# Kernel optimization log

Hardware: AMD Instinct MI355X
Metric: run time of the kernel (lower is better)

## Reference

```python
import jax, jax.numpy as jnp
import numpy as np

N = 4096        # number of sparse voxel tokens (single sequence)
C = 1024        # channels
H = 16          # num_heads
D = C // H      # head_dim = 64
FREQ_DIM = D // 2 // 3   # 10 rotary freqs per spatial axis
PAD = D // 2 - 3 * FREQ_DIM  # 2 identity-padded complex pairs


def setup_inputs() -> dict:
    key = jax.random.key(0)
    ks = jax.random.split(key, 6)
    s_in = 1.0 / np.sqrt(C)
    x = jax.random.normal(ks[0], (N, C), jnp.float32)
    coords = jax.random.randint(ks[1], (N, 3), 0, 64, dtype=jnp.int32)
    W_qkv = jax.random.normal(ks[2], (C, 3 * C), jnp.float32) * s_in
    b_qkv = jnp.zeros((3 * C,), jnp.float32)
    gamma_q = jnp.ones((H, D), jnp.float32)
    gamma_k = jnp.ones((H, D), jnp.float32)
    W_out = jax.random.normal(ks[3], (C, C), jnp.float32) * s_in
    b_out = jnp.zeros((C,), jnp.float32)
    return {"x": x, "coords": coords, "W_qkv": W_qkv, "b_qkv": b_qkv,
            "gamma_q": gamma_q, "gamma_k": gamma_k, "W_out": W_out, "b_out": b_out}


def _rms_norm(t, gamma):
    # F.normalize(x, dim=-1) * gamma * sqrt(D), computed in fp32
    t = t.astype(jnp.float32)
    nrm = jnp.maximum(jnp.linalg.norm(t, axis=-1, keepdims=True), 1e-12)
    return (t / nrm) * gamma * np.float32(np.sqrt(D))


def _rope_phases(coords):
    # freqs: rope_freq[0] / rope_freq[1]**(i/freq_dim)
    freqs = 1.0 / (10000.0 ** (jnp.arange(FREQ_DIM, dtype=jnp.float32) / FREQ_DIM))
    ph = coords.astype(jnp.float32).reshape(-1)[:, None] * freqs   # [N*3, FREQ_DIM]
    ph = ph.reshape(N, 3 * FREQ_DIM)
    # pad with zero-phase (identity rotation) to head_dim//2
    cos = jnp.concatenate([jnp.cos(ph), jnp.ones((N, PAD), jnp.float32)], axis=-1)
    sin = jnp.concatenate([jnp.sin(ph), jnp.zeros((N, PAD), jnp.float32)], axis=-1)
    return cos, sin


def _rope_apply(t, cos, sin):
    # complex rotation on consecutive pairs of the head dim
    tr = t.reshape(N, H, D // 2, 2)
    t0, t1 = tr[..., 0], tr[..., 1]
    c, s = cos[:, None, :], sin[:, None, :]
    o0 = t0 * c - t1 * s
    o1 = t0 * s + t1 * c
    return jnp.stack([o0, o1], axis=-1).reshape(N, H, D)


def reference(x, coords, W_qkv, b_qkv, gamma_q, gamma_k, W_out, b_out):
    qkv = (x @ W_qkv + b_qkv).reshape(N, 3, H, D)
    q, k, v = qkv[:, 0], qkv[:, 1], qkv[:, 2]
    q = _rms_norm(q, gamma_q)
    k = _rms_norm(k, gamma_k)
    cos, sin = _rope_phases(coords)
    q = _rope_apply(q, cos, sin)
    k = _rope_apply(k, cos, sin)
    scores = jnp.einsum('nhd,mhd->hnm', q, k) / np.float32(np.sqrt(D))
    attn = jax.nn.softmax(scores, axis=-1)
    h = jnp.einsum('hnm,mhd->nhd', attn, v).reshape(N, C)
    return h @ W_out + b_out
```

## Files before the change

### kernel.cpp

```cpp
#include <hip/hip_runtime.h>

#define DEVI __device__ __forceinline__

typedef __attribute__((ext_vector_type(8))) short bf16x8;
typedef __attribute__((ext_vector_type(4))) float f32x4;
typedef __attribute__((ext_vector_type(16))) float f32x16;

DEVI ushort f2bf(float f) {
  union { float f; unsigned u; } v; v.f = f;
  unsigned u = v.u;
  unsigned r = (u + 0x7FFFu + ((u >> 16) & 1u)) >> 16;
  return (ushort)r;
}
DEVI float bf2f(ushort h) {
  union { unsigned u; float f; } v; v.u = ((unsigned)h) << 16;
  return v.f;
}
DEVI unsigned pkbf(float lo, float hi) {
  unsigned r;
  asm("v_cvt_pk_bf16_f32 %0, %1, %2" : "=v"(r) : "v"(lo), "v"(hi));
  return r;
}
DEVI float exp2v(float x) {
#if __has_builtin(__builtin_amdgcn_exp2f)
  return __builtin_amdgcn_exp2f(x);
#else
  return exp2f(x);
#endif
}

DEVI void gload_lds16(const ushort* g, ushort* l) {
  __builtin_amdgcn_global_load_lds((const __attribute__((address_space(1))) void*)g,
                                   (__attribute__((address_space(3))) void*)l, 16, 0, 0);
}

DEVI void xcd_swz(int& bx, int& by) {
  const int nx = gridDim.x;
  const int flat = blockIdx.x + blockIdx.y * nx;
  const int cpx = (nx * gridDim.y) >> 3;
  const int swz = (flat & 7) * cpx + (flat >> 3);
  bx = swz % nx;
  by = swz / nx;
}

__global__ __launch_bounds__(256) void prep(const float* __restrict__ x,
                                            ushort* __restrict__ xb,
                                            const float* __restrict__ Wq,
                                            ushort* __restrict__ wtq,
                                            const float* __restrict__ Wo,
                                            ushort* __restrict__ wto) {
  __shared__ ushort tile[64][65];
  const int bid = blockIdx.x, t = threadIdx.x;
  if (bid < 4096) {
    int i = bid * 256 + t;
    const float4 v = ((const float4*)x)[i];
    uint2 o;
    o.x = (unsigned)f2bf(v.x) | ((unsigned)f2bf(v.y) << 16);
    o.y = (unsigned)f2bf(v.z) | ((unsigned)f2bf(v.w) << 16);
    ((uint2*)xb)[i] = o;
    return;
  }
  const float* in;
  ushort* out;
  int R, Cc, bx, by;
  if (bid < 4864) {
    in = Wq; out = wtq; R = 1024; Cc = 3072;
    bx = (bid - 4096) % 48; by = (bid - 4096) / 48;
  } else {
    in = Wo; out = wto; R = 1024; Cc = 1024;
    bx = (bid - 4864) % 16; by = (bid - 4864) / 16;
  }
  const int r0 = by * 64, c0 = bx * 64;
  for (int i = 0; i < 16; ++i) {
    int rr = i * 4 + (t >> 6), cc = t & 63;
    tile[rr][cc] = f2bf(in[(size_t)(r0 + rr) * Cc + c0 + cc]);
  }
  __syncthreads();
  for (int i = 0; i < 16; ++i) {
    int cc = i * 4 + (t >> 6), rr = t & 63;
    out[(size_t)(c0 + cc) * R + r0 + rr] = tile[rr][cc];
  }
}

template<int EPI>
__global__ __launch_bounds__(256) void gemm_bt(const ushort* __restrict__ A,
                                               const ushort* __restrict__ Bt,
                                               const float* __restrict__ bias,
                                               void* __restrict__ outp,
                                               int M, int Nn, int K) {
  __shared__ ushort As[2][128 * 32];
  __shared__ ushort Bs[2][128 * 32];
  const int tid = threadIdx.x;
  const int w = tid >> 6, l = tid & 63;
  int bx, by;
  xcd_swz(bx, by);
  const int m0 = by * 128, n0 = bx * 128;
  const int wm = (w >> 1) * 64, wn = (w & 1) * 64;
  const int lc = l & 15, lg = l >> 4;

  f32x4 acc[4][4];
  for (int i = 0; i < 4; ++i)
    for (int j = 0; j < 4; ++j) acc[i][j] = (f32x4){0.f, 0.f, 0.f, 0.f};

  const int srow = w * 32 + (l >> 2);
  const int scol = (l & 3) * 8;
  const ushort* gA = A + (size_t)(m0 + srow) * K + scol;
  const ushort* gB = Bt + (size_t)(n0 + srow) * K + scol;

  for (int k0 = 0; k0 < K; k0 += 64) {
#pragma unroll
    for (int s = 0; s < 2; ++s) {
      gload_lds16(gA + k0 + 32 * s,                  &As[s][(w * 32 + 0) * 32]);
      gload_lds16(gA + k0 + 32 * s + (size_t)16 * K, &As[s][(w * 32 + 16) * 32]);
      gload_lds16(gB + k0 + 32 * s,                  &Bs[s][(w * 32 + 0) * 32]);
      gload_lds16(gB + k0 + 32 * s + (size_t)16 * K, &Bs[s][(w * 32 + 16) * 32]);
    }
    __syncthreads();
#pragma unroll
    for (int s = 0; s < 2; ++s) {
      bf16x8 af[4], bfr[4];
      for (int mi = 0; mi < 4; ++mi)
        af[mi] = *(const bf16x8*)(&As[s][(wm + mi * 16 + lc) * 32 + lg * 8]);
      for (int ni = 0; ni < 4; ++ni)
        bfr[ni] = *(const bf16x8*)(&Bs[s][(wn + ni * 16 + lc) * 32 + lg * 8]);
      for (int mi = 0; mi < 4; ++mi)
        for (int ni = 0; ni < 4; ++ni)
          acc[mi][ni] = __builtin_amdgcn_mfma_f32_16x16x32_bf16(af[mi], bfr[ni], acc[mi][ni], 0, 0, 0);
    }
    __syncthreads();
  }

  const int lr = lg * 4;
  if constexpr (EPI == 1) {
    float* O = (float*)outp;
    for (int ni = 0; ni < 4; ++ni) {
      int col = n0 + wn + ni * 16 + lc;
      float bv = bias[col];
      for (int mi = 0; mi < 4; ++mi)
        for (int r = 0; r < 4; ++r)
          O[(size_t)(m0 + wm + mi * 16 + lr + r) * Nn + col] = acc[mi][ni][r] + bv;
    }
  } else {
    ushort* O = (ushort*)outp;
    for (int ni = 0; ni < 4; ++ni) {
      int col = n0 + wn + ni * 16 + lc;
      float bv = bias[col];
      int grp = col >> 10;
      int hh = (col >> 6) & 15;
      int dd = col & 63;
      if (grp < 2) {
        size_t base = (size_t)grp * (16 * 4096 * 64) + (size_t)hh * (4096 * 64) + dd;
        for (int mi = 0; mi < 4; ++mi)
          for (int r = 0; r < 4; ++r) {
            int row = m0 + wm + mi * 16 + lr + r;
            O[base + (size_t)row * 64] = f2bf(acc[mi][ni][r] + bv);
          }
      } else {
        size_t base = (size_t)2 * (16 * 4096 * 64) + ((size_t)hh * 64 + dd) * 4096;
        for (int mi = 0; mi < 4; ++mi)
          for (int r = 0; r < 4; ++r) {
            int row = m0 + wm + mi * 16 + lr + r;
            O[base + row] = f2bf(acc[mi][ni][r] + bv);
          }
      }
    }
  }
}

DEVI void nr_one(ushort* B, const float* g, size_t base, int h, int l16,
                 float c0a, float s0a, float c1a, float s1a, float extra) {
  unsigned u0 = *(const unsigned*)(B + base + 2 * l16);
  unsigned u1 = *(const unsigned*)(B + base + 32 + 2 * l16);
  float t00 = bf2f((ushort)u0), t01 = bf2f((ushort)(u0 >> 16));
  float t10 = bf2f((ushort)u1), t11 = bf2f((ushort)(u1 >> 16));
  float ss = t00 * t00 + t01 * t01 + t10 * t10 + t11 * t11;
  for (int d = 1; d < 16; d <<= 1) ss += __shfl_xor(ss, d, 16);
  float scl = 8.f / fmaxf(sqrtf(ss), 1e-12f);
  scl *= extra;
  float g00 = g[h * 64 + 2 * l16], g01 = g[h * 64 + 2 * l16 + 1];
  float g10 = g[h * 64 + 32 + 2 * l16], g11 = g[h * 64 + 33 + 2 * l16];
  float q00 = t00 * scl * g00, q01 = t01 * scl * g01;
  float q10 = t10 * scl * g10, q11 = t11 * scl * g11;
  float o00 = q00 * c0a - q01 * s0a, o01 = q00 * s0a + q01 * c0a;
  float o10 = q10 * c1a - q11 * s1a, o11 = q10 * s1a + q11 * c1a;
  *(unsigned*)(B + base + 2 * l16) = (unsigned)f2bf(o00) | ((unsigned)f2bf(o01) << 16);
  *(unsigned*)(B + base + 32 + 2 * l16) = (unsigned)f2bf(o10) | ((unsigned)f2bf(o11) << 16);
}

__global__ __launch_bounds__(256) void norm_rope(ushort* __restrict__ Qb,
                                                 ushort* __restrict__ Kb,
                                                 const int* __restrict__ coords,
                                                 const float* __restrict__ gq,
                                                 const float* __restrict__ gk) {
  const int n = blockIdx.x, t = threadIdx.x;
  const int h = t >> 4, l16 = t & 15;
  const float L2_10K_D10 = 1.3287712379549449f;
  float c0a, s0a, c1a, s1a;
  {
    int p = l16;
    int j = p / 10, fi = p - j * 10;
    float freq = exp2f(-(float)fi * L2_10K_D10);
    float ang = (float)coords[n * 3 + j] * freq;
    c0a = cosf(ang); s0a = sinf(ang);
  }
  {
    int p = l16 + 16;
    if (p < 30) {
      int j = p / 10, fi = p - j * 10;
      float freq = exp2f(-(float)fi * L2_10K_D10);
      float ang = (float)coords[n * 3 + j] * freq;
      c1a = cosf(ang); s1a = sinf(ang);
    } else { c1a = 1.f; s1a = 0.f; }
  }
  const size_t base = ((size_t)h * 4096 + n) * 64;
  nr_one(Qb, gq, base, h, l16, c0a, s0a, c1a, s1a, 0.125f * 1.4426950408889634f);
  nr_one(Kb, gk, base, h, l16, c0a, s0a, c1a, s1a, 1.0f);
}

DEVI void attn_step(const bf16x8 (&ck)[8], const bf16x8 (&cv)[8], const bf16x8 (&qf)[4],
                    f32x16& o0, f32x16& o1, f32x4& rs) {
  f32x16 s0, s1;
#pragma unroll
  for (int r = 0; r < 16; ++r) { s0[r] = 0.f; s1[r] = 0.f; }
#pragma unroll
  for (int c = 0; c < 4; ++c) {
    s0 = __builtin_amdgcn_mfma_f32_32x32x16_bf16(ck[c],     qf[c], s0, 0, 0, 0);
    s1 = __builtin_amdgcn_mfma_f32_32x32x16_bf16(ck[c + 4], qf[c], s1, 0, 0, 0);
  }
#pragma unroll
  for (int r = 0; r < 16; ++r) { s0[r] = exp2v(s0[r]); }
#pragma unroll
  for (int r = 0; r < 16; ++r) { s1[r] = exp2v(s1[r]); }
#pragma unroll
  for (int r = 0; r < 16; r += 4) {
    rs[0] += s0[r] + s1[r];
    rs[1] += s0[r + 1] + s1[r + 1];
    rs[2] += s0[r + 2] + s1[r + 2];
    rs[3] += s0[r + 3] + s1[r + 3];
  }
  union { unsigned u[4]; bf16x8 v; } pb[4];
  {
    auto r0 = __builtin_amdgcn_permlane32_swap(pkbf(s0[0], s0[1]), pkbf(s0[4], s0[5]), false, false);
    auto r1 = __builtin_amdgcn_permlane32_swap(pkbf(s0[2], s0[3]), pkbf(s0[6], s0[7]), false, false);
    pb[0].u[0] = r0[0]; pb[0].u[1] = r1[0]; pb[0].u[2] = r0[1]; pb[0].u[3] = r1[1];
    auto r2 = __builtin_amdgcn_permlane32_swap(pkbf(s0[8], s0[9]), pkbf(s0[12], s0[13]), false, false);
    auto r3 = __builtin_amdgcn_permlane32_swap(pkbf(s0[10], s0[11]), pkbf(s0[14], s0[15]), false, false);
    pb[1].u[0] = r2[0]; pb[1].u[1] = r3[0]; pb[1].u[2] = r2[1]; pb[1].u[3] = r3[1];
    auto r4 = __builtin_amdgcn_permlane32_swap(pkbf(s1[0], s1[1]), pkbf(s1[4], s1[5]), false, false);
    auto r5 = __builtin_amdgcn_permlane32_swap(pkbf(s1[2], s1[3]), pkbf(s1[6], s1[7]), false, false);
    pb[2].u[0] = r4[0]; pb[2].u[1] = r5[0]; pb[2].u[2] = r4[1]; pb[2].u[3] = r5[1];
    auto r6 = __builtin_amdgcn_permlane32_swap(pkbf(s1[8], s1[9]), pkbf(s1[12], s1[13]), false, false);
    auto r7 = __builtin_amdgcn_permlane32_swap(pkbf(s1[10], s1[11]), pkbf(s1[14], s1[15]), false, false);
    pb[3].u[0] = r6[0]; pb[3].u[1] = r7[0]; pb[3].u[2] = r6[1]; pb[3].u[3] = r7[1];
  }
#pragma unroll
  for (int c = 0; c < 4; ++c) {
    o0 = __builtin_amdgcn_mfma_f32_32x32x16_bf16(cv[c],     pb[c].v, o0, 0, 0, 0);
    o1 = __builtin_amdgcn_mfma_f32_32x32x16_bf16(cv[c + 4], pb[c].v, o1, 0, 0, 0);
  }
}

__global__ __launch_bounds__(256, 2) void attn_fwd(const ushort* __restrict__ Qb,
                                                   const ushort* __restrict__ Kb,
                                                   const ushort* __restrict__ Vt,
                                                   ushort* __restrict__ attnb) {
  __shared__ ushort Ks[2][4096];
  __shared__ ushort Vs[2][4096];

  const int flat = blockIdx.x + (blockIdx.y << 5);
  const int swz = (flat & 7) * 64 + (flat >> 3);
  const int bx = swz & 31, h = swz >> 5;

  const int l = threadIdx.x & 63, w = threadIdx.x >> 6;
  const int q = l & 31, hi = l >> 5;
  const int q0 = bx * 128 + w * 32;

  const ushort* qrow = Qb + ((size_t)h * 4096 + q0 + q) * 64 + hi * 8;
  bf16x8 qf[4];
#pragma unroll
  for (int c = 0; c < 4; ++c) qf[c] = *(const bf16x8*)(qrow + 16 * c);

  f32x16 o0, o1;
#pragma unroll
  for (int r = 0; r < 16; ++r) { o0[r] = 0.f; o1[r] = 0.f; }
  f32x4 rs = (f32x4){0.f, 0.f, 0.f, 0.f};

  const ushort* gK = Kb + ((size_t)h * 4096 + l) * 64 + 2 * w * 8;
  const ushort* gV = Vt + ((size_t)h * 64 + l) * 4096 + 2 * w * 8;

  ushort* Kc = &Ks[0][0]; ushort* Vc = &Vs[0][0];
  ushort* Kn = &Ks[1][0]; ushort* Vn = &Vs[1][0];

  gload_lds16(gK, Kc + 2 * w * 512);
  gload_lds16(gK + 8, Kc + (2 * w + 1) * 512);
  gload_lds16(gV, Vc + 2 * w * 512);
  gload_lds16(gV + 8, Vc + (2 * w + 1) * 512);
  asm volatile("s_waitcnt vmcnt(0)" ::: "memory");
  __builtin_amdgcn_s_barrier();
  __builtin_amdgcn_sched_barrier(0);

  const int lbase = hi * 512 + q * 8;
  for (int t = 0; t < 63; ++t) {
    const ushort* sK = gK + (size_t)(t + 1) * 64 * 64;
    const ushort* sV = gV + (t + 1) * 64;
    gload_lds16(sK, Kn + 2 * w * 512);
    gload_lds16(sK + 8, Kn + (2 * w + 1) * 512);
    gload_lds16(sV, Vn + 2 * w * 512);
    gload_lds16(sV + 8, Vn + (2 * w + 1) * 512);

    bf16x8 k[8], v[8];
#pragma unroll
    for (int c = 0; c < 4; ++c) {
      k[c]     = *(const bf16x8*)(Kc + lbase + c * 1024);
      k[c + 4] = *(const bf16x8*)(Kc + lbase + c * 1024 + 256);
      v[c]     = *(const bf16x8*)(Vc + lbase + c * 1024);
      v[c + 4] = *(const bf16x8*)(Vc + lbase + c * 1024 + 256);
    }
    __builtin_amdgcn_s_setprio(1);
    attn_step(k, v, qf, o0, o1, rs);
    __builtin_amdgcn_s_setprio(0);

    asm volatile("s_waitcnt vmcnt(0) lgkmcnt(0)" ::: "memory");
    __builtin_amdgcn_s_barrier();
    __builtin_amdgcn_sched_barrier(0);
    ushort* tp;
    tp = Kc; Kc = Kn; Kn = tp;
    tp = Vc; Vc = Vn; Vn = tp;
  }
  {
    bf16x8 k[8], v[8];
#pragma unroll
    for (int c = 0; c < 4; ++c) {
      k[c]     = *(const bf16x8*)(Kc + lbase + c * 1024);
      k[c + 4] = *(const bf16x8*)(Kc + lbase + c * 1024 + 256);
      v[c]     = *(const bf16x8*)(Vc + lbase + c * 1024);
      v[c + 4] = *(const bf16x8*)(Vc + lbase + c * 1024 + 256);
    }
    attn_step(k, v, qf, o0, o1, rs);
  }

  float lsum = (rs[0] + rs[1]) + (rs[2] + rs[3]);
  lsum += __shfl_xor(lsum, 32);
  const float inv = 1.f / lsum;
  ushort* orow = attnb + (size_t)(q0 + q) * 1024 + h * 64;
#pragma unroll
  for (int dt = 0; dt < 2; ++dt) {
    const f32x16& oo = dt ? o1 : o0;
#pragma unroll
    for (int g = 0; g < 4; ++g)
#pragma unroll
      for (int p2 = 0; p2 < 2; ++p2) {
        int r = g * 4 + p2 * 2;
        unsigned pk = pkbf(oo[r] * inv, oo[r + 1] * inv);
        *(unsigned*)(orow + dt * 32 + g * 8 + 4 * hi + p2 * 2) = pk;
      }
  }
}

extern "C" void kernel_launch(void* const* d_in, const int* in_sizes, int n_in,
                              void* d_out, int out_size, void* d_ws, size_t ws_size,
                              hipStream_t stream) {
  const float* x      = (const float*)d_in[0];
  const int*   coords = (const int*)d_in[1];
  const float* W_qkv  = (const float*)d_in[2];
  const float* b_qkv  = (const float*)d_in[3];
  const float* gq     = (const float*)d_in[4];
  const float* gk     = (const float*)d_in[5];
  const float* W_out  = (const float*)d_in[6];
  const float* b_out  = (const float*)d_in[7];
  float* out = (float*)d_out;

  char* ws = (char*)d_ws;
  ushort* xb    = (ushort*)(ws);
  ushort* wtqkv = (ushort*)(ws + (8u << 20));
  ushort* wtout = (ushort*)(ws + (14u << 20));
  ushort* Qb    = (ushort*)(ws + (16u << 20));
  ushort* Kb    = (ushort*)(ws + (24u << 20));
  ushort* Vt    = (ushort*)(ws + (32u << 20));
  ushort* attnb = (ushort*)(ws + (40u << 20));

  prep<<<5120, 256, 0, stream>>>(x, xb, W_qkv, wtqkv, W_out, wtout);
  gemm_bt<0><<<dim3(24, 32), 256, 0, stream>>>(xb, wtqkv, b_qkv, (void*)Qb, 4096, 3072, 1024);
  norm_rope<<<4096, 256, 0, stream>>>(Qb, Kb, coords, gq, gk);
  attn_fwd<<<dim3(32, 16), 256, 0, stream>>>(Qb, Kb, Vt, attnb);
  gemm_bt<1><<<dim3(8, 32), 256, 0, stream>>>(attnb, wtout, b_out, (void*)out, 4096, 1024, 1024);
}
```

Baseline: 158.6 us.

## Fuse QK RMS-norm and RoPE into QKV GEMM epilogue

Removes the separate norm_rope kernel and applies RMS normalization, gamma, softmax scale and rotary embedding inside the QKV GEMM epilogue. Each wave's 64-column tile covers exactly one head, so the per-row sum of squares is reduced with 16-lane shuffles and RoPE pairs are exchanged with a lane xor. This saves a kernel launch and a full read and write of Q and K. In exchange the epilogue recomputes sin/cos per element, loads coords per row, and adds more shuffles and register pressure to the GEMM.

```diff
diff --git a/kernel.cpp b/kernel.cpp
--- a/kernel.cpp
+++ b/kernel.cpp
@@ -87,7 +87,10 @@
                                                const ushort* __restrict__ Bt,
                                                const float* __restrict__ bias,
                                                void* __restrict__ outp,
-                                               int M, int Nn, int K) {
+                                               int M, int Nn, int K,
+                                               const int* __restrict__ coords,
+                                               const float* __restrict__ gq,
+                                               const float* __restrict__ gk) {
   __shared__ ushort As[2][128 * 32];
   __shared__ ushort Bs[2][128 * 32];
   const int tid = threadIdx.x;
@@ -142,79 +145,68 @@
     }
   } else {
     ushort* O = (ushort*)outp;
-    for (int ni = 0; ni < 4; ++ni) {
-      int col = n0 + wn + ni * 16 + lc;
-      float bv = bias[col];
-      int grp = col >> 10;
-      int hh = (col >> 6) & 15;
-      int dd = col & 63;
-      if (grp < 2) {
-        size_t base = (size_t)grp * (16 * 4096 * 64) + (size_t)hh * (4096 * 64) + dd;
-        for (int mi = 0; mi < 4; ++mi)
-          for (int r = 0; r < 4; ++r) {
-            int row = m0 + wm + mi * 16 + lr + r;
-            O[base + (size_t)row * 64] = f2bf(acc[mi][ni][r] + bv);
+    const int col0 = n0 + wn;
+    const int grp = col0 >> 10;
+    const int hh = (col0 >> 6) & 15;
+    if (grp < 2) {
+      const float extra = (grp == 0) ? 0.125f * 1.4426950408889634f : 1.0f;
+      const float* g = (grp == 0) ? gq : gk;
+      const float L2_10K_D10 = 1.3287712379549449f;
+      float gam[4], bv[4], cfreq[4];
+      int cj[4];
+#pragma unroll
+      for (int ni = 0; ni < 4; ++ni) {
+        gam[ni] = g[hh * 64 + ni * 16 + lc];
+        bv[ni] = bias[col0 + ni * 16 + lc];
+        int p = ni * 8 + (lc >> 1);
+        int j = p / 10, fi = p - 10 * j;
+        cj[ni] = j;
+        cfreq[ni] = (p < 30) ? exp2f(-(float)fi * L2_10K_D10) : 0.f;
+      }
+      const size_t hbase = (size_t)grp * (16 * 4096 * 64) + (size_t)hh * (4096 * 64);
+#pragma unroll
+      for (int mi = 0; mi < 4; ++mi)
+#pragma unroll
+        for (int r = 0; r < 4; ++r) {
+          const int row = m0 + wm + mi * 16 + lr + r;
+          float v[4];
+          float ss = 0.f;
+#pragma unroll
+          for (int ni = 0; ni < 4; ++ni) {
+            v[ni] = acc[mi][ni][r] + bv[ni];
+            ss += v[ni] * v[ni];
           }
-      } else {
+          ss += __shfl_xor(ss, 1, 16);
+          ss += __shfl_xor(ss, 2, 16);
+          ss += __shfl_xor(ss, 4, 16);
+          ss += __shfl_xor(ss, 8, 16);
+          const float scl = extra * 8.f / fmaxf(sqrtf(ss), 1e-12f);
+          const int c0 = coords[row * 3], c1 = coords[row * 3 + 1], c2 = coords[row * 3 + 2];
+#pragma unroll
+          for (int ni = 0; ni < 4; ++ni) {
+            float te = v[ni] * scl * gam[ni];
+            float po = __shfl_xor(te, 1);
+            int cc = cj[ni] == 0 ? c0 : (cj[ni] == 1 ? c1 : c2);
+            float ang = (float)cc * cfreq[ni];
+            float cs = cosf(ang), sn = sinf(ang);
+            float outv = (lc & 1) ? po * sn + te * cs : te * cs - po * sn;
+            O[hbase + (size_t)row * 64 + ni * 16 + lc] = f2bf(outv);
+          }
+        }
+    } else {
+      for (int ni = 0; ni < 4; ++ni) {
+        int col = col0 + ni * 16 + lc;
+        float bvv = bias[col];
+        int dd = col & 63;
         size_t base = (size_t)2 * (16 * 4096 * 64) + ((size_t)hh * 64 + dd) * 4096;
         for (int mi = 0; mi < 4; ++mi)
           for (int r = 0; r < 4; ++r) {
             int row = m0 + wm + mi * 16 + lr + r;
-            O[base + row] = f2bf(acc[mi][ni][r] + bv);
+            O[base + row] = f2bf(acc[mi][ni][r] + bvv);
           }
       }
     }
   }
-}
-
-DEVI void nr_one(ushort* B, const float* g, size_t base, int h, int l16,
-                 float c0a, float s0a, float c1a, float s1a, float extra) {
-  unsigned u0 = *(const unsigned*)(B + base + 2 * l16);
-  unsigned u1 = *(const unsigned*)(B + base + 32 + 2 * l16);
-  float t00 = bf2f((ushort)u0), t01 = bf2f((ushort)(u0 >> 16));
-  float t10 = bf2f((ushort)u1), t11 = bf2f((ushort)(u1 >> 16));
-  float ss = t00 * t00 + t01 * t01 + t10 * t10 + t11 * t11;
-  for (int d = 1; d < 16; d <<= 1) ss += __shfl_xor(ss, d, 16);
-  float scl = 8.f / fmaxf(sqrtf(ss), 1e-12f);
-  scl *= extra;
-  float g00 = g[h * 64 + 2 * l16], g01 = g[h * 64 + 2 * l16 + 1];
-  float g10 = g[h * 64 + 32 + 2 * l16], g11 = g[h * 64 + 33 + 2 * l16];
-  float q00 = t00 * scl * g00, q01 = t01 * scl * g01;
-  float q10 = t10 * scl * g10, q11 = t11 * scl * g11;
-  float o00 = q00 * c0a - q01 * s0a, o01 = q00 * s0a + q01 * c0a;
-  float o10 = q10 * c1a - q11 * s1a, o11 = q10 * s1a + q11 * c1a;
-  *(unsigned*)(B + base + 2 * l16) = (unsigned)f2bf(o00) | ((unsigned)f2bf(o01) << 16);
-  *(unsigned*)(B + base + 32 + 2 * l16) = (unsigned)f2bf(o10) | ((unsigned)f2bf(o11) << 16);
-}
-
-__global__ __launch_bounds__(256) void norm_rope(ushort* __restrict__ Qb,
-                                                 ushort* __restrict__ Kb,
-                                                 const int* __restrict__ coords,
-                                                 const float* __restrict__ gq,
-                                                 const float* __restrict__ gk) {
-  const int n = blockIdx.x, t = threadIdx.x;
-  const int h = t >> 4, l16 = t & 15;
-  const float L2_10K_D10 = 1.3287712379549449f;
-  float c0a, s0a, c1a, s1a;
-  {
-    int p = l16;
-    int j = p / 10, fi = p - j * 10;
-    float freq = exp2f(-(float)fi * L2_10K_D10);
-    float ang = (float)coords[n * 3 + j] * freq;
-    c0a = cosf(ang); s0a = sinf(ang);
-  }
-  {
-    int p = l16 + 16;
-    if (p < 30) {
-      int j = p / 10, fi = p - j * 10;
-      float freq = exp2f(-(float)fi * L2_10K_D10);
-      float ang = (float)coords[n * 3 + j] * freq;
-      c1a = cosf(ang); s1a = sinf(ang);
-    } else { c1a = 1.f; s1a = 0.f; }
-  }
-  const size_t base = ((size_t)h * 4096 + n) * 64;
-  nr_one(Qb, gq, base, h, l16, c0a, s0a, c1a, s1a, 0.125f * 1.4426950408889634f);
-  nr_one(Kb, gk, base, h, l16, c0a, s0a, c1a, s1a, 1.0f);
 }
 
 DEVI void attn_step(const bf16x8 (&ck)[8], const bf16x8 (&cv)[8], const bf16x8 (&qf)[4],
@@ -380,8 +372,9 @@
   ushort* attnb = (ushort*)(ws + (40u << 20));
 
   prep<<<5120, 256, 0, stream>>>(x, xb, W_qkv, wtqkv, W_out, wtout);
-  gemm_bt<0><<<dim3(24, 32), 256, 0, stream>>>(xb, wtqkv, b_qkv, (void*)Qb, 4096, 3072, 1024);
-  norm_rope<<<4096, 256, 0, stream>>>(Qb, Kb, coords, gq, gk);
+  gemm_bt<0><<<dim3(24, 32), 256, 0, stream>>>(xb, wtqkv, b_qkv, (void*)Qb, 4096, 3072, 1024,
+                                               coords, gq, gk);
   attn_fwd<<<dim3(32, 16), 256, 0, stream>>>(Qb, Kb, Vt, attnb);
-  gemm_bt<1><<<dim3(8, 32), 256, 0, stream>>>(attnb, wtout, b_out, (void*)out, 4096, 1024, 1024);
-}
+  gemm_bt<1><<<dim3(8, 32), 256, 0, stream>>>(attnb, wtout, b_out, (void*)out, 4096, 1024, 1024,
+                                              nullptr, nullptr, nullptr);
+}
```

After: 282.4 us. +78.0%, slower.

## Add dedicated 256x192-tile QKV GEMM kernel with swizzled LDS and wider K steps

Applied to the files above, without the earlier changes.

Replaces the generic 128x128 templated GEMM for the QKV projection with a specialized kernel. It uses 512 threads, 256x192 tiles (exactly 256 blocks), a K step of 64, an XOR-swizzled LDS layout to avoid bank conflicts, explicit waitcnt/barrier double buffering, s_setprio around the MFMA bursts, and an XCD-aware block swizzle. The aim is more data reuse per block and fewer LDS conflicts and barriers per FLOP, at the cost of higher register and LDS pressure (about 112KB LDS). The output GEMM keeps the old design as a non-template kernel.

```diff
diff --git a/kernel.cpp b/kernel.cpp
--- a/kernel.cpp
+++ b/kernel.cpp
@@ -82,12 +82,122 @@
   }
 }
 
-template<int EPI>
-__global__ __launch_bounds__(256) void gemm_bt(const ushort* __restrict__ A,
-                                               const ushort* __restrict__ Bt,
-                                               const float* __restrict__ bias,
-                                               void* __restrict__ outp,
-                                               int M, int Nn, int K) {
+__global__ __launch_bounds__(512, 2) void gemm_qkv(const ushort* __restrict__ A,
+                                                   const ushort* __restrict__ Bt,
+                                                   const float* __restrict__ bias,
+                                                   ushort* __restrict__ O) {
+  __shared__ ushort lds[2 * 28672];
+  const int tid = threadIdx.x;
+  const int w = tid >> 6, l = tid & 63;
+  const int flat = blockIdx.x;
+  const int swz = (flat & 7) * 32 + (flat >> 3);
+  const int bm = swz >> 4, bn = swz & 15;
+  const int m0 = bm * 256, n0 = bn * 192;
+  const int wm = (w >> 2) * 128, wn = (w & 3) * 48;
+  const int lc = l & 15, lg = l >> 4;
+
+  const int lrow = l >> 3;
+  const int lcol = ((l & 7) ^ lrow) * 8;
+  const ushort* pA[4];
+  const ushort* pB[3];
+#pragma unroll
+  for (int i = 0; i < 4; ++i)
+    pA[i] = A + (size_t)(m0 + (w * 4 + i) * 8 + lrow) * 1024 + lcol;
+#pragma unroll
+  for (int i = 0; i < 3; ++i)
+    pB[i] = Bt + (size_t)(n0 + (w * 3 + i) * 8 + lrow) * 1024 + lcol;
+
+  ushort* cur = lds;
+  ushort* nxt = lds + 28672;
+
+#pragma unroll
+  for (int i = 0; i < 4; ++i) gload_lds16(pA[i], cur + (w * 4 + i) * 512);
+#pragma unroll
+  for (int i = 0; i < 3; ++i) gload_lds16(pB[i], cur + 16384 + (w * 3 + i) * 512);
+  asm volatile("s_waitcnt vmcnt(0)" ::: "memory");
+  __builtin_amdgcn_s_barrier();
+  __builtin_amdgcn_sched_barrier(0);
+
+  f32x4 acc[8][3];
+#pragma unroll
+  for (int i = 0; i < 8; ++i)
+#pragma unroll
+    for (int j = 0; j < 3; ++j) acc[i][j] = (f32x4){0.f, 0.f, 0.f, 0.f};
+
+  const int aoff = (wm + lc) * 64;
+  const int boff = 16384 + (wn + lc) * 64;
+  const int roph0 = ((0 + lg) ^ (lc & 7)) * 8;
+  const int roph1 = ((4 + lg) ^ (lc & 7)) * 8;
+
+  for (int t = 0; t < 16; ++t) {
+    if (t < 15) {
+#pragma unroll
+      for (int i = 0; i < 4; ++i) gload_lds16(pA[i] + (t + 1) * 64, nxt + (w * 4 + i) * 512);
+#pragma unroll
+      for (int i = 0; i < 3; ++i) gload_lds16(pB[i] + (t + 1) * 64, nxt + 16384 + (w * 3 + i) * 512);
+    }
+    bf16x8 bfr[2][3];
+#pragma unroll
+    for (int fc = 0; fc < 3; ++fc) {
+      bfr[0][fc] = *(const bf16x8*)(cur + boff + fc * 1024 + roph0);
+      bfr[1][fc] = *(const bf16x8*)(cur + boff + fc * 1024 + roph1);
+    }
+    __builtin_amdgcn_s_setprio(1);
+#pragma unroll
+    for (int kc = 0; kc < 2; ++kc) {
+      const int roph = kc ? roph1 : roph0;
+      bf16x8 af[8];
+#pragma unroll
+      for (int fr = 0; fr < 8; ++fr)
+        af[fr] = *(const bf16x8*)(cur + aoff + fr * 1024 + roph);
+#pragma unroll
+      for (int fr = 0; fr < 8; ++fr)
+#pragma unroll
+        for (int fc = 0; fc < 3; ++fc)
+          acc[fr][fc] = __builtin_amdgcn_mfma_f32_16x16x32_bf16(af[fr], bfr[kc][fc], acc[fr][fc], 0, 0, 0);
+    }
+    __builtin_amdgcn_s_setprio(0);
+    if (t < 15) {
+      asm volatile("s_waitcnt vmcnt(0) lgkmcnt(0)" ::: "memory");
+      __builtin_amdgcn_s_barrier();
+      __builtin_amdgcn_sched_barrier(0);
+      ushort* tp = cur; cur = nxt; nxt = tp;
+    }
+  }
+
+  const int lr = lg * 4;
+#pragma unroll
+  for (int fc = 0; fc < 3; ++fc) {
+    const int col = n0 + wn + fc * 16 + lc;
+    const float bv = bias[col];
+    const int grp = col >> 10, hh = (col >> 6) & 15, dd = col & 63;
+    if (grp < 2) {
+      size_t base = (size_t)grp * (16 * 4096 * 64) + (size_t)hh * (4096 * 64) + dd;
+#pragma unroll
+      for (int fr = 0; fr < 8; ++fr)
+#pragma unroll
+        for (int r = 0; r < 4; ++r) {
+          int row = m0 + wm + fr * 16 + lr + r;
+          O[base + (size_t)row * 64] = f2bf(acc[fr][fc][r] + bv);
+        }
+    } else {
+      size_t base = (size_t)2 * (16 * 4096 * 64) + ((size_t)hh * 64 + dd) * 4096;
+#pragma unroll
+      for (int fr = 0; fr < 8; ++fr)
+#pragma unroll
+        for (int r = 0; r < 4; ++r) {
+          int row = m0 + wm + fr * 16 + lr + r;
+          O[base + row] = f2bf(acc[fr][fc][r] + bv);
+        }
+    }
+  }
+}
+
+__global__ __launch_bounds__(256) void gemm_out(const ushort* __restrict__ A,
+                                                const ushort* __restrict__ Bt,
+                                                const float* __restrict__ bias,
+                                                float* __restrict__ O,
+                                                int M, int Nn, int K) {
   __shared__ ushort As[2][128 * 32];
   __shared__ ushort Bs[2][128 * 32];
   const int tid = threadIdx.x;
@@ -131,39 +241,12 @@
   }
 
   const int lr = lg * 4;
-  if constexpr (EPI == 1) {
-    float* O = (float*)outp;
-    for (int ni = 0; ni < 4; ++ni) {
-      int col = n0 + wn + ni * 16 + lc;
-      float bv = bias[col];
-      for (int mi = 0; mi < 4; ++mi)
-        for (int r = 0; r < 4; ++r)
-          O[(size_t)(m0 + wm + mi * 16 + lr + r) * Nn + col] = acc[mi][ni][r] + bv;
-    }
-  } else {
-    ushort* O = (ushort*)outp;
-    for (int ni = 0; ni < 4; ++ni) {
-      int col = n0 + wn + ni * 16 + lc;
-      float bv = bias[col];
-      int grp = col >> 10;
-      int hh = (col >> 6) & 15;
-      int dd = col & 63;
-      if (grp < 2) {
-        size_t base = (size_t)grp * (16 * 4096 * 64) + (size_t)hh * (4096 * 64) + dd;
-        for (int mi = 0; mi < 4; ++mi)
-          for (int r = 0; r < 4; ++r) {
-            int row = m0 + wm + mi * 16 + lr + r;
-            O[base + (size_t)row * 64] = f2bf(acc[mi][ni][r] + bv);
-          }
-      } else {
-        size_t base = (size_t)2 * (16 * 4096 * 64) + ((size_t)hh * 64 + dd) * 4096;
-        for (int mi = 0; mi < 4; ++mi)
-          for (int r = 0; r < 4; ++r) {
-            int row = m0 + wm + mi * 16 + lr + r;
-            O[base + row] = f2bf(acc[mi][ni][r] + bv);
-          }
-      }
-    }
+  for (int ni = 0; ni < 4; ++ni) {
+    int col = n0 + wn + ni * 16 + lc;
+    float bv = bias[col];
+    for (int mi = 0; mi < 4; ++mi)
+      for (int r = 0; r < 4; ++r)
+        O[(size_t)(m0 + wm + mi * 16 + lr + r) * Nn + col] = acc[mi][ni][r] + bv;
   }
 }
 
@@ -380,8 +463,8 @@
   ushort* attnb = (ushort*)(ws + (40u << 20));
 
   prep<<<5120, 256, 0, stream>>>(x, xb, W_qkv, wtqkv, W_out, wtout);
-  gemm_bt<0><<<dim3(24, 32), 256, 0, stream>>>(xb, wtqkv, b_qkv, (void*)Qb, 4096, 3072, 1024);
+  gemm_qkv<<<256, 512, 0, stream>>>(xb, wtqkv, b_qkv, Qb);
   norm_rope<<<4096, 256, 0, stream>>>(Qb, Kb, coords, gq, gk);
   attn_fwd<<<dim3(32, 16), 256, 0, stream>>>(Qb, Kb, Vt, attnb);
-  gemm_bt<1><<<dim3(8, 32), 256, 0, stream>>>(attnb, wtout, b_out, (void*)out, 4096, 1024, 1024);
-}
+  gemm_out<<<dim3(8, 32), 256, 0, stream>>>(attnb, wtout, b_out, out, 4096, 1024, 1024);
+}
```

New measurement: 153.9 us. -3.0%, faster.
